# Performance work log

Hardware: AMD Instinct MI355X
Metric: run time of the kernel (lower is better)

The kernel has to match this reference:

```python
import jax, jax.numpy as jnp
import numpy as np

NUM_BITS = 10
D_MODEL = 256
D_INNER = 512                      # expand=2 * hidden
D_STATE = 64
N_HEADS = 8                        # D_INNER // head_dim(64)
HEAD_DIM = 64
CONV_DIM = D_INNER + 2 * D_STATE   # 640
D_PROJ = D_INNER + CONV_DIM + N_HEADS  # 1160
KERNEL = 4
EPS = 1e-5
N_TOKENS = 16384


def _hilbert_code(coords):
    # coords: (N,3) int32 in [0, 2**NUM_BITS); Skilling's AxesToTranspose + bit interleave
    n = 3
    x = [coords[:, i] for i in range(n)]
    M = 1 << (NUM_BITS - 1)
    Q = M
    while Q > 1:
        P = Q - 1
        for i in range(n):
            cond = (x[i] & Q) > 0
            t = (x[0] ^ x[i]) & P
            x0_new = jnp.where(cond, x[0] ^ P, x[0] ^ t)
            xi_new = jnp.where(cond, x[i], x[i] ^ t)
            x[0] = x0_new
            if i > 0:
                x[i] = xi_new
        Q >>= 1
    for i in range(1, n):
        x[i] = x[i] ^ x[i - 1]
    t = jnp.zeros_like(x[0])
    Q = M
    while Q > 1:
        t = jnp.where((x[n - 1] & Q) > 0, t ^ (Q - 1), t)
        Q >>= 1
    x = [xi ^ t for xi in x]
    code = jnp.zeros_like(x[0])
    for b in range(NUM_BITS - 1, -1, -1):
        for i in range(n):
            code = (code << 1) | ((x[i] >> b) & 1)
    return code


def _serialized_orders(query_pos):
    # quantize to a 2**NUM_BITS grid, Hilbert-encode, sort ('hilbert' and 'hilbert-trans' = x/y swapped)
    pmin = query_pos.min(0)
    pmax = query_pos.max(0)
    g = ((query_pos - pmin) / (pmax - pmin + 1e-6) * (2 ** NUM_BITS - 1))
    g = jnp.clip(g, 0, 2 ** NUM_BITS - 1).astype(jnp.int32)
    orders, inverses = [], []
    for perm in ((0, 1, 2), (1, 0, 2)):
        code = _hilbert_code(g[:, jnp.array(perm)])
        o = jnp.argsort(code)
        orders.append(o)
        inverses.append(jnp.argsort(o))
    return orders, inverses


def _ln(x, w, b):
    m = x.mean(-1, keepdims=True)
    xc = x - m
    return xc * jax.lax.rsqrt(jnp.mean(xc * xc, -1, keepdims=True) + EPS) * w + b


def _mamba2(x, p):
    # x: (B, L, D_MODEL)
    B, L, _ = x.shape
    zxbcdt = x @ p['in_proj']                           # (B,L,1160)
    gate = zxbcdt[..., :D_INNER]
    xBC = zxbcdt[..., D_INNER:D_INNER + CONV_DIM]
    dt = zxbcdt[..., D_INNER + CONV_DIM:]               # (B,L,H)
    # causal depthwise conv over time
    xc = jnp.moveaxis(xBC, -1, 1)                       # (B,C,L)
    xc = jax.lax.conv_general_dilated(
        xc, p['conv_w'][:, None, :], window_strides=(1,),
        padding=[(KERNEL - 1, 0)], dimension_numbers=('NCH', 'OIH', 'NCH'),
        feature_group_count=CONV_DIM)
    xc = xc + p['conv_b'][None, :, None]
    xBC = jax.nn.silu(jnp.moveaxis(xc, 1, -1))          # (B,L,C)
    xs = xBC[..., :D_INNER].reshape(B, L, N_HEADS, HEAD_DIM)
    Bm = xBC[..., D_INNER:D_INNER + D_STATE]            # (B,L,S), n_groups=1 broadcast over heads
    Cm = xBC[..., D_INNER + D_STATE:]                   # (B,L,S)
    dt = jax.nn.softplus(dt + p['dt_bias'])             # (B,L,H)
    A = -jnp.exp(p['A_log'])                            # (H,)
    dA = jnp.exp(dt * A)                                # (B,L,H)

    def step(h, inp):
        dA_t, dt_t, x_t, B_t, C_t = inp                 # (B,H),(B,H),(B,H,P),(B,S),(B,S)
        h = h * dA_t[..., None, None] + (dt_t[..., None] * x_t)[..., None] * B_t[:, None, None, :]
        y = jnp.einsum('bhps,bs->bhp', h, C_t)
        return h, y

    tm = lambda a: jnp.moveaxis(a, 1, 0)
    h0 = jnp.zeros((B, N_HEADS, HEAD_DIM, D_STATE), x.dtype)
    _, ys = jax.lax.scan(step, h0, (tm(dA), tm(dt), tm(xs), tm(Bm), tm(Cm)))
    y = jnp.moveaxis(ys, 0, 1) + p['D'][None, None, :, None] * xs   # (B,L,H,P) + D skip
    y = y.reshape(B, L, D_INNER)
    # gated RMSNorm (MambaRMSNormGated)
    y = y * jax.nn.silu(gate)
    y = y * jax.lax.rsqrt(jnp.mean(y * y, -1, keepdims=True) + EPS) * p['norm_w']
    return y @ p['out_proj']                            # (B,L,D_MODEL)


def _forward(query, query_pos, pre_w, pre_b, fin_w, fin_b, layer_params):
    orders, invs = _serialized_orders(query_pos)
    q = query
    for p in layer_params:
        shortcut = q
        qn = _ln(q, pre_w, pre_b)
        stacked = jnp.stack([qn[orders[0]], qn[orders[1]]])   # (2, N, d) multi-path serialization
        y = _mamba2(stacked, p)
        q = shortcut + (y[0][invs[0]] + y[1][invs[1]]) * 0.5  # scatter back + average paths
        q = _ln(q, fin_w, fin_b)
    return q


def setup_inputs() -> dict:
    key = jax.random.key(0)
    ks = jax.random.split(key, 24)
    inp = {
        'query': jax.random.normal(ks[0], (N_TOKENS, D_MODEL), jnp.float32),
        'query_pos': jax.random.uniform(ks[1], (N_TOKENS, 3), jnp.float32),
        'pre_w': jnp.ones((D_MODEL,), jnp.float32),
        'pre_b': jnp.zeros((D_MODEL,), jnp.float32),
        'fin_w': jnp.ones((D_MODEL,), jnp.float32),
        'fin_b': jnp.zeros((D_MODEL,), jnp.float32),
    }
    for i in range(2):
        k = jax.random.split(ks[2 + i], 6)
        inp[f'in_proj{i}'] = jax.random.normal(k[0], (D_MODEL, D_PROJ), jnp.float32) * 0.02
        inp[f'conv_w{i}'] = jax.random.normal(k[1], (CONV_DIM, KERNEL), jnp.float32) * 0.2
        inp[f'conv_b{i}'] = jnp.zeros((CONV_DIM,), jnp.float32)
        inp[f'dt_bias{i}'] = jax.random.uniform(k[2], (N_HEADS,), jnp.float32, -4.0, -1.0)
        inp[f'A_log{i}'] = jnp.log(jnp.arange(1, N_HEADS + 1, dtype=jnp.float32))
        inp[f'D{i}'] = jnp.ones((N_HEADS,), jnp.float32)
        inp[f'norm_w{i}'] = jnp.ones((D_INNER,), jnp.float32)
        inp[f'out_proj{i}'] = jax.random.normal(k[3], (D_INNER, D_MODEL), jnp.float32) * 0.02
    return inp


def reference(query, query_pos, pre_w, pre_b, fin_w, fin_b,
              in_proj0, conv_w0, conv_b0, dt_bias0, A_log0, D0, norm_w0, out_proj0,
              in_proj1, conv_w1, conv_b1, dt_bias1, A_log1, D1, norm_w1, out_proj1):
    layer_params = [
        dict(in_proj=in_proj0, conv_w=conv_w0, conv_b=conv_b0, dt_bias=dt_bias0,
             A_log=A_log0, D=D0, norm_w=norm_w0, out_proj=out_proj0),
        dict(in_proj=in_proj1, conv_w=conv_w1, conv_b=conv_b1, dt_bias=dt_bias1,
             A_log=A_log1, D=D1, norm_w=norm_w1, out_proj=out_proj1),
    ]
    return _forward(query, query_pos, pre_w, pre_b, fin_w, fin_b, layer_params)
```

## Files before the change

### kernel.cpp

```cpp
#include <hip/hip_runtime.h>
#include <stdint.h>

#define L_TOK 16384
#define DM 256
#define DI 512
#define DS 64
#define NH 8
#define HD 64
#define CD 640
#define DP 1160
#define CHUNK 64
#define NC 256
#define EPSF 1e-5f

typedef __attribute__((ext_vector_type(8))) short short8;
typedef __attribute__((ext_vector_type(4))) float f32x4;

#define GLL16(gp, lp) __builtin_amdgcn_global_load_lds((const __attribute__((address_space(1))) void*)(gp), (__attribute__((address_space(3))) void*)(lp), 16, 0, 0)

__device__ __forceinline__ float warp_sum(float v) {
  v += __shfl_xor(v, 1, 64);
  v += __shfl_xor(v, 2, 64);
  v += __shfl_xor(v, 4, 64);
  v += __shfl_xor(v, 8, 64);
  v += __shfl_xor(v, 16, 64);
  v += __shfl_xor(v, 32, 64);
  return v;
}

__device__ __forceinline__ float fexp(float x) { return __expf(x); }
__device__ __forceinline__ float fsilu(float x) { return x * __builtin_amdgcn_rcpf(1.0f + __expf(-x)); }
__device__ __forceinline__ float siluf(float x) { return x / (1.0f + expf(-x)); }

__device__ __forceinline__ unsigned short f2bf(float f) {
  unsigned int u = __float_as_uint(f);
  unsigned int r = (u + 0x7FFFu + ((u >> 16) & 1u)) >> 16;
  return (unsigned short)r;
}
__device__ __forceinline__ float bf2f(unsigned short u) {
  return __uint_as_float(((unsigned int)u) << 16);
}


__global__ __launch_bounds__(256) void minmax_part(const float* __restrict__ pos, float* __restrict__ part) {
  __shared__ float sm[6][4];
  int tid = threadIdx.x;
  int t = blockIdx.x*256 + tid;
  float a = pos[t*3+0], b = pos[t*3+1], c = pos[t*3+2];
  float mn0=a, mn1=b, mn2=c, mx0=a, mx1=b, mx2=c;
  #pragma unroll
  for (int d = 1; d < 64; d <<= 1) {
    mn0=fminf(mn0,__shfl_xor(mn0,d,64));
    mn1=fminf(mn1,__shfl_xor(mn1,d,64));
    mn2=fminf(mn2,__shfl_xor(mn2,d,64));
    mx0=fmaxf(mx0,__shfl_xor(mx0,d,64));
    mx1=fmaxf(mx1,__shfl_xor(mx1,d,64));
    mx2=fmaxf(mx2,__shfl_xor(mx2,d,64));
  }
  if ((tid & 63) == 0) {
    int w = tid >> 6;
    sm[0][w]=mn0; sm[1][w]=mn1; sm[2][w]=mn2;
    sm[3][w]=mx0; sm[4][w]=mx1; sm[5][w]=mx2;
  }
  __syncthreads();
  if (tid < 6) {
    float r = sm[tid][0];
    if (tid < 3) { r=fminf(r,sm[tid][1]); r=fminf(r,sm[tid][2]); r=fminf(r,sm[tid][3]); }
    else         { r=fmaxf(r,sm[tid][1]); r=fmaxf(r,sm[tid][2]); r=fmaxf(r,sm[tid][3]); }
    part[blockIdx.x*6 + tid] = r;
  }
}

__global__ __launch_bounds__(64) void minmax_final(const float* __restrict__ part, float* __restrict__ pmm) {
  int tid = threadIdx.x;
  const float* p = part + tid*6;
  float mn0=p[0], mn1=p[1], mn2=p[2], mx0=p[3], mx1=p[4], mx2=p[5];
  #pragma unroll
  for (int d = 1; d < 64; d <<= 1) {
    mn0=fminf(mn0,__shfl_xor(mn0,d,64));
    mn1=fminf(mn1,__shfl_xor(mn1,d,64));
    mn2=fminf(mn2,__shfl_xor(mn2,d,64));
    mx0=fmaxf(mx0,__shfl_xor(mx0,d,64));
    mx1=fmaxf(mx1,__shfl_xor(mx1,d,64));
    mx2=fmaxf(mx2,__shfl_xor(mx2,d,64));
  }
  if (tid == 0) {
    pmm[0]=mn0; pmm[1]=mn1; pmm[2]=mn2;
    pmm[3]=mx0; pmm[4]=mx1; pmm[5]=mx2;
  }
}

__device__ unsigned int hilbert3(unsigned int a, unsigned int b, unsigned int c) {
  unsigned int x0 = a, x1 = b, x2 = c;
  for (unsigned int Q = 512u; Q > 1u; Q >>= 1) {
    unsigned int P = Q - 1u;
    { if (x0 & Q) x0 ^= P; }
    {
      unsigned int t = (x0 ^ x1) & P;
      if (x1 & Q) { x0 ^= P; }
      else { x0 ^= t; x1 ^= t; }
    }
    {
      unsigned int t = (x0 ^ x2) & P;
      if (x2 & Q) { x0 ^= P; }
      else { x0 ^= t; x2 ^= t; }
    }
  }
  x1 ^= x0; x2 ^= x1;
  unsigned int tt = 0;
  for (unsigned int Q = 512u; Q > 1u; Q >>= 1)
    if (x2 & Q) tt ^= (Q - 1u);
  x0 ^= tt; x1 ^= tt; x2 ^= tt;
  unsigned int code = 0;
  #pragma unroll
  for (int bb = 9; bb >= 0; --bb) {
    code = (code << 1) | ((x0 >> bb) & 1u);
    code = (code << 1) | ((x1 >> bb) & 1u);
    code = (code << 1) | ((x2 >> bb) & 1u);
  }
  return code;
}

__global__ __launch_bounds__(256) void hilbert_kernel(const float* __restrict__ pos, const float* __restrict__ pmm,
                                                      unsigned long long* __restrict__ keys) {
  int t = blockIdx.x*256 + threadIdx.x;
  if (t >= L_TOK) return;
  unsigned int g[3];
  #pragma unroll
  for (int d = 0; d < 3; ++d) {
    float v = (pos[t*3+d] - pmm[d]) / (pmm[3+d] - pmm[d] + 1e-6f) * 1023.0f;
    v = fminf(fmaxf(v, 0.0f), 1023.0f);
    g[d] = (unsigned int)(int)v;
  }
  unsigned int ca = hilbert3(g[0], g[1], g[2]);
  unsigned int cb = hilbert3(g[1], g[0], g[2]);
  keys[t]         = ((unsigned long long)ca << 14) | (unsigned long long)t;
  keys[L_TOK + t] = ((unsigned long long)cb << 14) | (unsigned long long)t;
}

__global__ __launch_bounds__(256) void rank_partial(const unsigned long long* __restrict__ keys,
                                                    unsigned int* __restrict__ partial) {
  __shared__ unsigned long long tile[512];
  int arr = blockIdx.y, ks = blockIdx.z;
  const unsigned long long* k = keys + (size_t)arr * L_TOK;
  int qbase = blockIdx.x*1024 + threadIdx.x;
  unsigned long long q[4];
  #pragma unroll
  for (int i = 0; i < 4; ++i) q[i] = k[qbase + 256*i];
  const unsigned long long* src = k + ks*512;
  #pragma unroll
  for (int t = 0; t < 2; ++t) tile[threadIdx.x + 256*t] = src[threadIdx.x + 256*t];
  __syncthreads();
  unsigned int r[4] = {};
  const ulonglong2* t2 = (const ulonglong2*)tile;
  #pragma unroll 4
  for (int j = 0; j < 256; ++j) {
    ulonglong2 v = t2[j];
    #pragma unroll
    for (int i = 0; i < 4; ++i) {
      r[i] += (v.x < q[i]) ? 1u : 0u;
      r[i] += (v.y < q[i]) ? 1u : 0u;
    }
  }
  #pragma unroll
  for (int i = 0; i < 4; ++i)
    partial[(size_t)(ks*2 + arr)*L_TOK + qbase + 256*i] = r[i];
}

__global__ __launch_bounds__(256) void rank_scatter(const unsigned long long* __restrict__ keys,
                                                    const unsigned int* __restrict__ partial,
                                                    unsigned int* __restrict__ ord,
                                                    unsigned int* __restrict__ inv) {
  int i = blockIdx.x*256 + threadIdx.x;
  int arr = i >> 14;
  int qi = i & (L_TOK - 1);
  unsigned int r = 0;
  #pragma unroll
  for (int ks = 0; ks < 32; ++ks) r += partial[(size_t)(ks*2 + arr)*L_TOK + qi];
  unsigned int tok = (unsigned int)(keys[i] & 0x3FFFu);
  ord[(size_t)arr*L_TOK + r] = tok;
  inv[(size_t)arr*L_TOK + tok] = r;
}


__global__ __launch_bounds__(256) void ln_kernel(const float* __restrict__ in, float* __restrict__ out,
                                                 unsigned short* __restrict__ outbf,
                                                 const float* __restrict__ w, const float* __restrict__ b) {
  int row = blockIdx.x*4 + (threadIdx.x >> 6);
  int lane = threadIdx.x & 63;
  const float4 v = *(const float4*)(in + (size_t)row*DM + lane*4);
  float s = v.x + v.y + v.z + v.w;
  float mean = warp_sum(s) * (1.0f/DM);
  float4 xc = make_float4(v.x-mean, v.y-mean, v.z-mean, v.w-mean);
  float ss = xc.x*xc.x + xc.y*xc.y + xc.z*xc.z + xc.w*xc.w;
  ss = warp_sum(ss) * (1.0f/DM);
  float inv = rsqrtf(ss + EPSF);
  const float4 w4 = *(const float4*)(w + lane*4);
  const float4 b4 = *(const float4*)(b + lane*4);
  float4 o;
  o.x = xc.x*inv*w4.x + b4.x;
  o.y = xc.y*inv*w4.y + b4.y;
  o.z = xc.z*inv*w4.z + b4.z;
  o.w = xc.w*inv*w4.w + b4.w;
  *(float4*)(out + (size_t)row*DM + lane*4) = o;
  if (outbf) {
    ushort4 ob = make_ushort4(f2bf(o.x), f2bf(o.y), f2bf(o.z), f2bf(o.w));
    *(ushort4*)(outbf + (size_t)row*DM + lane*4) = ob;
  }
}

__global__ __launch_bounds__(256) void lnfuse_kernel(float* __restrict__ io,
                                                     float* __restrict__ qn, unsigned short* __restrict__ qnbf,
                                                     const float* __restrict__ fw, const float* __restrict__ fb,
                                                     const float* __restrict__ pw, const float* __restrict__ pb) {
  int row = blockIdx.x*4 + (threadIdx.x >> 6);
  int lane = threadIdx.x & 63;
  const float4 v = *(const float4*)(io + (size_t)row*DM + lane*4);
  float s = v.x + v.y + v.z + v.w;
  float mean = warp_sum(s) * (1.0f/DM);
  float4 xc = make_float4(v.x-mean, v.y-mean, v.z-mean, v.w-mean);
  float ss = xc.x*xc.x + xc.y*xc.y + xc.z*xc.z + xc.w*xc.w;
  ss = warp_sum(ss) * (1.0f/DM);
  float inv = rsqrtf(ss + EPSF);
  const float4 w4 = *(const float4*)(fw + lane*4);
  const float4 b4 = *(const float4*)(fb + lane*4);
  float4 o;
  o.x = xc.x*inv*w4.x + b4.x;
  o.y = xc.y*inv*w4.y + b4.y;
  o.z = xc.z*inv*w4.z + b4.z;
  o.w = xc.w*inv*w4.w + b4.w;
  *(float4*)(io + (size_t)row*DM + lane*4) = o;
  if (qn) {
    float s2 = o.x + o.y + o.z + o.w;
    float mean2 = warp_sum(s2) * (1.0f/DM);
    float4 x2 = make_float4(o.x-mean2, o.y-mean2, o.z-mean2, o.w-mean2);
    float ss2 = x2.x*x2.x + x2.y*x2.y + x2.z*x2.z + x2.w*x2.w;
    ss2 = warp_sum(ss2) * (1.0f/DM);
    float inv2 = rsqrtf(ss2 + EPSF);
    const float4 pw4 = *(const float4*)(pw + lane*4);
    const float4 pb4 = *(const float4*)(pb + lane*4);
    float4 qv;
    qv.x = x2.x*inv2*pw4.x + pb4.x;
    qv.y = x2.y*inv2*pw4.y + pb4.y;
    qv.z = x2.z*inv2*pw4.z + pb4.z;
    qv.w = x2.w*inv2*pw4.w + pb4.w;
    *(float4*)(qn + (size_t)row*DM + lane*4) = qv;
    ushort4 qb = make_ushort4(f2bf(qv.x), f2bf(qv.y), f2bf(qv.z), f2bf(qv.w));
    *(ushort4*)(qnbf + (size_t)row*DM + lane*4) = qb;
  }
}


__global__ __launch_bounds__(256) void tcvt_both(const float* __restrict__ Wi, const float* __restrict__ Wo,
                                                 const float* __restrict__ nw,
                                                 unsigned short* __restrict__ WtA, unsigned short* __restrict__ WtO) {
  int idx = blockIdx.x*256 + threadIdx.x;
  if (idx < 1152*DM) {
    int n = idx >> 8, k = idx & 255;
    WtA[idx] = f2bf(Wi[(size_t)k*DP + n]);
  } else {
    int j = idx - 1152*DM;
    int n = j >> 9, k = j & 511;
    WtO[j] = f2bf(Wo[(size_t)k*DM + n] * nw[k]);
  }
}


__global__ __launch_bounds__(256) void gemm_in2(const unsigned short* __restrict__ Abf,
                                                const unsigned short* __restrict__ Wt,
                                                const unsigned int* __restrict__ ord,
                                                unsigned short* __restrict__ gate_nat,
                                                unsigned short* __restrict__ bcraw,
                                                unsigned short* __restrict__ xTg) {
  __shared__ unsigned short Alds[128*64];
  __shared__ unsigned short Blds[128*64];
  int tid = threadIdx.x, lane = tid & 63, w = tid >> 6;
  int bid = blockIdx.x;
  bool natp = bid < 640;
  int rb, cb, dir = 0, wcol0;
  if (natp) {
    int xcd = bid & 7, g = bid >> 3;
    rb = (xcd*16 + g/5)*128;
    cb = (g % 5)*128;
    wcol0 = cb;
  } else {
    int id = bid - 640;
    dir = id >> 9;
    int b = id & 511;
    int xcd = b & 7, g = b >> 3;
    rb = (xcd*16 + g/4)*128;
    cb = (g % 4)*128;
    wcol0 = DI + cb;
  }
  int wm = (w & 1)*64, wn = (w >> 1)*64;
  const unsigned int* ordp = ord + (size_t)dir*L_TOK;
  const unsigned short* pA[4]; const unsigned short* pB[4];
  unsigned short* dA[4]; unsigned short* dB[4];
  #pragma unroll
  for (int s = 0; s < 4; ++s) {
    int inst = w*4 + s;
    int r = inst*8 + (lane >> 3);
    int cA = (lane & 7) ^ (r & 7);
    int arow = natp ? (rb + r) : (int)ordp[rb + r];
    pA[s] = Abf + (size_t)arow*DM + cA*8;
    pB[s] = Wt + (size_t)(wcol0 + r)*DM + cA*8;
    dA[s] = &Alds[inst*512];
    dB[s] = &Blds[inst*512];
  }
  f32x4 zero = {0.f, 0.f, 0.f, 0.f};
  f32x4 acc[4][4];
  #pragma unroll
  for (int i = 0; i < 4; ++i)
    #pragma unroll
    for (int j = 0; j < 4; ++j) acc[i][j] = zero;
  int t = lane & 15, q = lane >> 4;
  for (int k0 = 0; k0 < DM; k0 += 64) {
    #pragma unroll
    for (int s = 0; s < 4; ++s) GLL16(pA[s] + k0, dA[s]);
    #pragma unroll
    for (int s = 0; s < 4; ++s) GLL16(pB[s] + k0, dB[s]);
    __syncthreads();
    #pragma unroll
    for (int ks = 0; ks < 2; ++ks) {
      short8 af[4], bfr[4];
      int cc = ks*4 + q;
      #pragma unroll
      for (int i = 0; i < 4; ++i) {
        int rr = wm + 16*i + t;
        af[i] = *(const short8*)&Alds[rr*64 + ((cc ^ (rr & 7))*8)];
      }
      #pragma unroll
      for (int j = 0; j < 4; ++j) {
        int rr = wn + 16*j + t;
        bfr[j] = *(const short8*)&Blds[rr*64 + ((cc ^ (rr & 7))*8)];
      }
      #pragma unroll
      for (int i = 0; i < 4; ++i)
        #pragma unroll
        for (int j = 0; j < 4; ++j)
          acc[i][j] = __builtin_amdgcn_mfma_f32_16x16x32_bf16(af[i], bfr[j], acc[i][j], 0, 0, 0);
    }
    __syncthreads();
  }
  if (natp) {
    unsigned short* dst; int ld;
    if (cb < DI) { dst = gate_nat + cb; ld = DI; }
    else         { dst = bcraw + (cb - DI); ld = 128; }
    #pragma unroll
    for (int i = 0; i < 4; ++i) {
      int rowb = rb + wm + 16*i + q*4;
      #pragma unroll
      for (int j = 0; j < 4; ++j) {
        int col = wn + 16*j + t;
        #pragma unroll
        for (int r = 0; r < 4; ++r)
          dst[(size_t)(rowb + r)*ld + col] = f2bf(acc[i][j][r]);
      }
    }
  } else {
    #pragma unroll
    for (int i = 0; i < 4; ++i) {
      int rowb = rb + wm + 16*i + q*4;
      #pragma unroll
      for (int j = 0; j < 4; ++j) {
        int col = wn + 16*j + t;
        ushort4 o = make_ushort4(f2bf(acc[i][j][0]), f2bf(acc[i][j][1]),
                                 f2bf(acc[i][j][2]), f2bf(acc[i][j][3]));
        *(ushort4*)(xTg + (size_t)(cb + col)*(2*L_TOK) + (size_t)dir*L_TOK + rowb) = o;
      }
    }
  }
}


__global__ __launch_bounds__(256) void gemm_out_gather(const unsigned short* __restrict__ ybuf,
                                                       const unsigned short* __restrict__ Wt,
                                                       const unsigned int* __restrict__ inv,
                                                       const float* __restrict__ rms_acc,
                                                       const float* __restrict__ shortcut,
                                                       float* __restrict__ out) {
  __shared__ unsigned short Alds[2*64*64];
  __shared__ unsigned short Blds[128*64];
  int tid = threadIdx.x, lane = tid & 63, w = tid >> 6;
  int bid = blockIdx.x;
  int xcd = bid & 7, g = bid >> 3;
  int rb = (xcd*32 + (g >> 1))*64;
  int cb = (g & 1)*128;
  int wm = (w & 1)*32, wn = (w >> 1)*64;
  const unsigned short* pA0[2]; const unsigned short* pA1[2];
  unsigned short* dA0[2]; unsigned short* dA1[2];
  const unsigned short* pB[4]; unsigned short* dB[4];
  #pragma unroll
  for (int s = 0; s < 2; ++s) {
    int inst = w*2 + s;
    int r = inst*8 + (lane >> 3);
    int cA = (lane & 7) ^ (r & 7);
    int tok = rb + r;
    pA0[s] = ybuf + (size_t)inv[tok]*DI + cA*8;
    pA1[s] = ybuf + (size_t)L_TOK*DI + (size_t)inv[L_TOK + tok]*DI + cA*8;
    dA0[s] = &Alds[inst*512];
    dA1[s] = &Alds[4096 + inst*512];
  }
  #pragma unroll
  for (int s = 0; s < 4; ++s) {
    int inst = w*4 + s;
    int r = inst*8 + (lane >> 3);
    int cA = (lane & 7) ^ (r & 7);
    pB[s] = Wt + (size_t)(cb + r)*DI + cA*8;
    dB[s] = &Blds[inst*512];
  }
  f32x4 zero = {0.f, 0.f, 0.f, 0.f};
  f32x4 acc0[2][4], acc1[2][4];
  #pragma unroll
  for (int i = 0; i < 2; ++i)
    #pragma unroll
    for (int j = 0; j < 4; ++j) { acc0[i][j] = zero; acc1[i][j] = zero; }
  int t = lane & 15, q = lane >> 4;
  for (int k0 = 0; k0 < DI; k0 += 64) {
    #pragma unroll
    for (int s = 0; s < 2; ++s) { GLL16(pA0[s] + k0, dA0[s]); GLL16(pA1[s] + k0, dA1[s]); }
    #pragma unroll
    for (int s = 0; s < 4; ++s) GLL16(pB[s] + k0, dB[s]);
    __syncthreads();
    #pragma unroll
    for (int ks = 0; ks < 2; ++ks) {
      short8 af0[2], af1[2], bfr[4];
      int cc = ks*4 + q;
      #pragma unroll
      for (int i = 0; i < 2; ++i) {
        int rr = wm + 16*i + t;
        int off = rr*64 + ((cc ^ (rr & 7))*8);
        af0[i] = *(const short8*)&Alds[off];
        af1[i] = *(const short8*)&Alds[4096 + off];
      }
      #pragma unroll
      for (int j = 0; j < 4; ++j) {
        int rr = wn + 16*j + t;
        bfr[j] = *(const short8*)&Blds[rr*64 + ((cc ^ (rr & 7))*8)];
      }
      #pragma unroll
      for (int i = 0; i < 2; ++i)
        #pragma unroll
        for (int j = 0; j < 4; ++j) {
          acc0[i][j] = __builtin_amdgcn_mfma_f32_16x16x32_bf16(af0[i], bfr[j], acc0[i][j], 0, 0, 0);
          acc1[i][j] = __builtin_amdgcn_mfma_f32_16x16x32_bf16(af1[i], bfr[j], acc1[i][j], 0, 0, 0);
        }
    }
    __syncthreads();
  }
  #pragma unroll
  for (int i = 0; i < 2; ++i) {
    #pragma unroll
    for (int r = 0; r < 4; ++r) {
      int row = rb + wm + 16*i + q*4 + r;
      float ir0 = rsqrtf(rms_acc[row]*(1.0f/DI) + EPSF);
      float ir1 = rsqrtf(rms_acc[L_TOK + row]*(1.0f/DI) + EPSF);
      const float* sp = shortcut + (size_t)row*DM + cb;
      float* op = out + (size_t)row*DM + cb;
      #pragma unroll
      for (int j = 0; j < 4; ++j) {
        int col = wn + 16*j + t;
        op[col] = sp[col] + 0.5f*(ir0*acc0[i][j][r] + ir1*acc1[i][j][r]);
      }
    }
  }
}


__global__ __launch_bounds__(256) void dtconv(const float* __restrict__ qn, const float* __restrict__ W,
                                              const float* __restrict__ dt_bias, float* __restrict__ dtb,
                                              float* __restrict__ rms_acc,
                                              const unsigned short* __restrict__ bcraw,
                                              const float* __restrict__ cw, const float* __restrict__ cbias,
                                              const unsigned int* __restrict__ ord,
                                              unsigned short* __restrict__ bcswz,
                                              unsigned short* __restrict__ bcswzA) {
  __shared__ unsigned short smem[131*64];
  int tid = threadIdx.x;
  int bx = blockIdx.x;
  if (bx < 512) {
    int gid = bx*256 + tid;
    if (gid < 2*L_TOK) rms_acc[gid] = 0.f;
    float* Wl = (float*)smem;
    {
      const float* wp = W + (size_t)tid*DP + (DI + CD);
      float4 wa = *(const float4*)wp;
      float4 wb = *(const float4*)(wp + 4);
      int off = tid*8 + (tid >> 5)*4;
      *(float4*)&Wl[off]     = wa;
      *(float4*)&Wl[off + 4] = wb;
    }
    __syncthreads();
    int lane = tid & 63, w = tid >> 6;
    int r = bx*32 + w*8 + (lane >> 3);
    int kg = lane & 7;
    const float* qp = qn + (size_t)r*DM + kg*32;
    float acc[8] = {};
    #pragma unroll
    for (int i = 0; i < 8; ++i) {
      float4 q4 = *(const float4*)(qp + i*4);
      float qv[4] = {q4.x, q4.y, q4.z, q4.w};
      #pragma unroll
      for (int e = 0; e < 4; ++e) {
        int k = kg*32 + i*4 + e;
        int off = k*8 + kg*4;
        float4 wa = *(const float4*)&Wl[off];
        float4 wb = *(const float4*)&Wl[off + 4];
        acc[0] = fmaf(qv[e], wa.x, acc[0]);
        acc[1] = fmaf(qv[e], wa.y, acc[1]);
        acc[2] = fmaf(qv[e], wa.z, acc[2]);
        acc[3] = fmaf(qv[e], wa.w, acc[3]);
        acc[4] = fmaf(qv[e], wb.x, acc[4]);
        acc[5] = fmaf(qv[e], wb.y, acc[5]);
        acc[6] = fmaf(qv[e], wb.z, acc[6]);
        acc[7] = fmaf(qv[e], wb.w, acc[7]);
      }
    }
    #pragma unroll
    for (int h = 0; h < 8; ++h) {
      acc[h] += __shfl_xor(acc[h], 8, 64);
      acc[h] += __shfl_xor(acc[h], 16, 64);
      acc[h] += __shfl_xor(acc[h], 32, 64);
    }
    float v = 0.f;
    #pragma unroll
    for (int h = 0; h < 8; ++h) if (kg == h) v = acc[h];
    v += dt_bias[kg];
    float sp = (v > 0.0f) ? (v + log1pf(__expf(-v))) : log1pf(__expf(v));
    dtb[(size_t)r*NH + kg] = sp;
  } else {
    int cid = bx - 512;
    int half = cid & 1, ty = (cid >> 1) & 127, dir = cid >> 8;
    unsigned short* tile = smem;
    const unsigned int* ordp = ord + (size_t)dir*L_TOK;
    int ch0 = DI + half*64;
    int co0 = half*64;
    int t0 = ty*128;
    for (int cc = tid; cc < 131*8; cc += 256) {
      int r = cc >> 3, cgc = cc & 7;
      int t = t0 - 3 + r;
      short8 v = {0,0,0,0,0,0,0,0};
      if (t >= 0) v = *(const short8*)(bcraw + (size_t)ordp[t]*128 + co0 + cgc*8);
      *(short8*)&tile[r*64 + ((cgc ^ (r & 7))*8)] = v;
    }
    int cg = tid & 7, tp = tid >> 3;
    int ch = ch0 + cg*8;
    float wv[8][4];
    float bias[8];
    #pragma unroll
    for (int e = 0; e < 8; ++e) {
      float4 c4 = *(const float4*)(cw + (ch + e)*4);
      wv[e][0] = c4.x; wv[e][1] = c4.y; wv[e][2] = c4.z; wv[e][3] = c4.w;
    }
    {
      float4 b0 = *(const float4*)(cbias + ch);
      float4 b1 = *(const float4*)(cbias + ch + 4);
      bias[0]=b0.x; bias[1]=b0.y; bias[2]=b0.z; bias[3]=b0.w;
      bias[4]=b1.x; bias[5]=b1.y; bias[6]=b1.z; bias[7]=b1.w;
    }
    __syncthreads();
    #pragma unroll
    for (int tk = 0; tk < 4; ++tk) {
      int rel = tp + 32*tk;
      float acc[8];
      #pragma unroll
      for (int e = 0; e < 8; ++e) acc[e] = bias[e];
      #pragma unroll
      for (int k = 0; k < 4; ++k) {
        int r = rel + k;
        short8 v = *(const short8*)&tile[r*64 + ((cg ^ (r & 7))*8)];
        #pragma unroll
        for (int e = 0; e < 8; ++e)
          acc[e] = fmaf(wv[e][k], bf2f((unsigned short)v[e]), acc[e]);
      }
      short8 o;
      #pragma unroll
      for (int e = 0; e < 8; ++e) o[e] = (short)f2bf(fsilu(acc[e]));
      int T = t0 + rel;
      int chn = T >> 6, tl = T & 63;
      unsigned short* tb = bcswz + ((size_t)((dir*NC + chn)*2 + half))*4096;
      *(short8*)(tb + tl*64 + ((cg ^ (tl & 7))*8)) = o;
      if (half == 0) {
        unsigned short* ta = bcswzA + ((size_t)(dir*NC + chn))*4096;
        #pragma unroll
        for (int e = 0; e < 8; ++e) {
          int s5 = cg*8 + e;
          ta[s5*64 + (((tl >> 3) ^ (s5 & 7))*8) + (tl & 7)] = (unsigned short)o[e];
        }
      }
    }
  }
}


__global__ __launch_bounds__(256) void phaseA_mfma(const unsigned short* __restrict__ xTg,
                                                   const unsigned short* __restrict__ bcswzA,
                                                   const float* __restrict__ cw, const float* __restrict__ cbias,
                                                   const float* __restrict__ dtb, const float* __restrict__ A_log,
                                                   const unsigned int* __restrict__ ord,
                                                   unsigned short* __restrict__ S, float* __restrict__ P,
                                                   unsigned short* __restrict__ xsT) {
  int c = blockIdx.x, h = blockIdx.y, dir = blockIdx.z, tid = threadIdx.x;
  int lane = tid & 63, w = tid >> 6;
  int hh = dir*NH + h;
  __shared__ unsigned short xT[64*64];
  __shared__ unsigned short Bt[64*64];
  __shared__ float wgt[64];
  int c0 = c*CHUNK;
  float Ah = -expf(A_log[h]);
  const unsigned short* bA = bcswzA + ((size_t)(dir*NC + c))*4096;
  #pragma unroll
  for (int s = 0; s < 2; ++s) {
    int inst = w*2 + s;
    GLL16(bA + (size_t)inst*512 + lane*8, &Bt[inst*512]);
  }
  if (tid < 64) {
    unsigned int tok = ord[(size_t)dir*L_TOK + c0 + tid];
    float dtv = dtb[(size_t)tok*NH + h];
    float v = dtv*Ah;
    float s = v;
    #pragma unroll
    for (int d = 1; d < 64; d <<= 1) {
      float u = __shfl_down(s, d, 64);
      s += (tid + d < 64) ? u : 0.f;
    }
    wgt[tid] = dtv*fexp(s - v);
    if (tid == 0) P[hh*NC + c] = fexp(s);
  }
  __syncthreads();
  unsigned short* xpg = xsT + ((size_t)(hh*NC + c))*4096;
  #pragma unroll
  for (int i = 0; i < 2; ++i) {
    int q = tid + 256*i;
    int p = q >> 3, tg = q & 7;
    int sw8 = (tg ^ (p & 7))*8;
    const unsigned short* xrow = xTg + (size_t)(h*HD + p)*(2*L_TOK) + (size_t)dir*L_TOK;
    int tb = c0 + tg*8;
    short8 cur = *(const short8*)(xrow + tb);
    short8 prv = {0,0,0,0,0,0,0,0};
    if (tb >= 8) prv = *(const short8*)(xrow + tb - 8);
    float4 w4 = *(const float4*)(cw + (size_t)(h*HD + p)*4);
    float bb = cbias[h*HD + p];
    float xv[11];
    xv[0] = bf2f((unsigned short)prv[5]);
    xv[1] = bf2f((unsigned short)prv[6]);
    xv[2] = bf2f((unsigned short)prv[7]);
    #pragma unroll
    for (int k = 0; k < 8; ++k) xv[3+k] = bf2f((unsigned short)cur[k]);
    short8 raw, wtd;
    #pragma unroll
    for (int k = 0; k < 8; ++k) {
      float a = bb + w4.x*xv[k] + w4.y*xv[k+1] + w4.z*xv[k+2] + w4.w*xv[k+3];
      unsigned short rbf = f2bf(fsilu(a));
      raw[k] = (short)rbf;
      wtd[k] = (short)f2bf(bf2f(rbf)*wgt[tg*8 + k]);
    }
    *(short8*)(xpg + p*64 + sw8) = raw;
    *(short8*)&xT[p*64 + sw8] = wtd;
  }
  __syncthreads();
  int t16 = lane & 15, q4 = lane >> 4;
  f32x4 zero = {0.f,0.f,0.f,0.f};
  f32x4 acc[4];
  #pragma unroll
  for (int j = 0; j < 4; ++j) acc[j] = zero;
  #pragma unroll
  for (int ks = 0; ks < 2; ++ks) {
    int rowA = 16*w + t16;
    short8 a = *(const short8*)&xT[rowA*64 + (((ks*4 + q4) ^ (rowA & 7))*8)];
    #pragma unroll
    for (int j = 0; j < 4; ++j) {
      int rowB = 16*j + t16;
      short8 b = *(const short8*)&Bt[rowB*64 + (((ks*4 + q4) ^ (rowB & 7))*8)];
      acc[j] = __builtin_amdgcn_mfma_f32_16x16x32_bf16(a, b, acc[j], 0, 0, 0);
    }
  }
  unsigned short* Sp = S + ((size_t)(hh*NC + c))*4096;
  #pragma unroll
  for (int j = 0; j < 4; ++j)
    #pragma unroll
    for (int r = 0; r < 4; ++r) {
      int row = 16*w + q4*4 + r;
      int cg2 = 2*j + (t16 >> 3);
      Sp[(size_t)row*64 + (((cg2 ^ (row & 7)) << 3) | (t16 & 7))] = f2bf(acc[j][r]);
    }
}


__global__ __launch_bounds__(128) void phaseB_scan(unsigned short* __restrict__ S, const float* __restrict__ P) {
  __shared__ float Pl[NC];
  int b = blockIdx.x;
  int hh = b >> 4;
  int e2 = (b & 15)*128 + threadIdx.x;
  for (int i = threadIdx.x; i < NC; i += 128) Pl[i] = P[hh*NC + i];
  __syncthreads();
  unsigned int* base = (unsigned int*)(S + ((size_t)hh*NC)*4096) + e2;
  float hx = 0.f, hy = 0.f;
  #pragma unroll 1
  for (int k0 = 0; k0 < NC; k0 += 16) {
    unsigned int v[16];
    #pragma unroll
    for (int u = 0; u < 16; ++u) v[u] = base[(size_t)(k0+u)*2048];
    #pragma unroll
    for (int u = 0; u < 16; ++u) {
      float p = Pl[k0+u];
      unsigned int old = v[u];
      base[(size_t)(k0+u)*2048] = (unsigned int)f2bf(hx) | ((unsigned int)f2bf(hy) << 16);
      hx = p*hx + bf2f((unsigned short)(old & 0xffffu));
      hy = p*hy + bf2f((unsigned short)(old >> 16));
    }
  }
}

__global__ __launch_bounds__(256) void phaseC_mfma(const unsigned short* __restrict__ bcswz,
                                                   const unsigned short* __restrict__ xsT,
                                                   const unsigned short* __restrict__ gate_nat,
                                                   const float* __restrict__ dtb, const float* __restrict__ A_log,
                                                   const float* __restrict__ Dp,
                                                   const unsigned int* __restrict__ ord,
                                                   const unsigned short* __restrict__ S,
                                                   unsigned short* __restrict__ ybuf,
                                                   float* __restrict__ rms_acc) {
  int c = blockIdx.x, h = blockIdx.y, dir = blockIdx.z, tid = threadIdx.x;
  int lane = tid & 63, w = tid >> 6;
  int hh = dir*NH + h;
  unsigned short* y = ybuf + (size_t)dir*L_TOK*DI;
  __shared__ __align__(16) unsigned short smemT[4*4096];
  __shared__ float dts[64], pl[64], pe[64];
  unsigned short* Cl  = smemT;
  unsigned short* Bl  = smemT + 4096;
  unsigned short* h0l = smemT + 8192;
  unsigned short* xT  = smemT + 12288;
  float* fT = (float*)(smemT + 8192);
  int c0 = c*CHUNK;
  float Ah = -expf(A_log[h]);
  float Dh = Dp[h];
  const unsigned short* Sp = S + ((size_t)(hh*NC + c))*4096;
  const unsigned short* xp = xsT + ((size_t)(hh*NC + c))*4096;
  const unsigned short* Bg = bcswz + ((size_t)((dir*NC + c)*2 + 0))*4096;
  const unsigned short* Cg = bcswz + ((size_t)((dir*NC + c)*2 + 1))*4096;
  #pragma unroll
  for (int s = 0; s < 2; ++s) {
    int inst = w*2 + s;
    GLL16(Sp + (size_t)inst*512 + lane*8, &h0l[inst*512]);
    GLL16(xp + (size_t)inst*512 + lane*8, &xT[inst*512]);
    GLL16(Bg + (size_t)inst*512 + lane*8, &Bl[inst*512]);
    GLL16(Cg + (size_t)inst*512 + lane*8, &Cl[inst*512]);
  }
  int erow = tid >> 2;
  int ech0 = (tid & 3) * 16;
  unsigned int etok = ord[(size_t)dir*L_TOK + c0 + erow];
  const unsigned short* gp = gate_nat + (size_t)etok*DI + h*HD + ech0;
  short8 g0 = *(const short8*)gp;
  short8 g1 = *(const short8*)(gp + 8);
  if (tid < 64) {
    unsigned int tok = ord[(size_t)dir*L_TOK + c0 + tid];
    float dtv = dtb[(size_t)tok*NH + h];
    dts[tid] = dtv;
    float v = dtv*Ah;
    float s = v;
    #pragma unroll
    for (int d = 1; d < 64; d <<= 1) {
      float u = __shfl_up(s, d, 64);
      s += (tid >= d) ? u : 0.f;
    }
    pl[tid] = s;
    pe[tid] = fexp(s);
  }
  __syncthreads();
  int t16 = lane & 15, q4 = lane >> 4;
  int t0 = 16*w;
  f32x4 zero = {0.f,0.f,0.f,0.f};
  f32x4 accG[4], accY[4];
  #pragma unroll
  for (int j = 0; j < 4; ++j) { accG[j] = zero; accY[j] = zero; }
  #pragma unroll
  for (int ks = 0; ks < 2; ++ks) {
    int rowA = t0 + t16;
    short8 a = *(const short8*)&Cl[rowA*64 + (((ks*4 + q4) ^ (rowA & 7))*8)];
    #pragma unroll
    for (int j = 0; j < 4; ++j) {
      int rowB = 16*j + t16;
      int off = rowB*64 + (((ks*4 + q4) ^ (rowB & 7))*8);
      accG[j] = __builtin_amdgcn_mfma_f32_16x16x32_bf16(a, *(const short8*)&Bl[off], accG[j], 0, 0, 0);
      accY[j] = __builtin_amdgcn_mfma_f32_16x16x32_bf16(a, *(const short8*)&h0l[off], accY[j], 0, 0, 0);
    }
  }
  #pragma unroll
  for (int j = 0; j < 4; ++j) {
    #pragma unroll
    for (int r = 0; r < 4; ++r) {
      int t = t0 + q4*4 + r;
      int s = 16*j + t16;
      float v = 0.f;
      if (s <= t) {
        v = accG[j][r] * dts[s] * fexp(pl[t] - pl[s]);
        if (s == t) v += Dh;
      }
      Cl[t*64 + (((s >> 3) ^ (t & 7))*8 + (s & 7))] = f2bf(v);
    }
  }
  #pragma unroll
  for (int j = 0; j < 4; ++j)
    #pragma unroll
    for (int r = 0; r < 4; ++r)
      accY[j][r] *= pe[t0 + q4*4 + r];
  #pragma unroll
  for (int ks = 0; ks < 2; ++ks) {
    int rowA = t0 + t16;
    short8 a = *(const short8*)&Cl[rowA*64 + (((ks*4 + q4) ^ (rowA & 7))*8)];
    #pragma unroll
    for (int j = 0; j < 4; ++j) {
      int rowB = 16*j + t16;
      short8 b = *(const short8*)&xT[rowB*64 + (((ks*4 + q4) ^ (rowB & 7))*8)];
      accY[j] = __builtin_amdgcn_mfma_f32_16x16x32_bf16(a, b, accY[j], 0, 0, 0);
    }
  }
  __syncthreads();
  #pragma unroll
  for (int j = 0; j < 4; ++j)
    #pragma unroll
    for (int r = 0; r < 4; ++r) {
      int t = t0 + q4*4 + r;
      int p = 16*j + t16;
      fT[t*64 + (p ^ (q4 << 4))] = accY[j][r];
    }
  __syncthreads();
  {
    int swz = ((erow >> 2) & 3) << 4;
    const float* fr = &fT[erow*64 + (ech0 ^ swz)];
    float4 a0 = *(const float4*)(fr);
    float4 a1 = *(const float4*)(fr + 4);
    float4 a2 = *(const float4*)(fr + 8);
    float4 a3 = *(const float4*)(fr + 12);
    float fv[16] = {a0.x,a0.y,a0.z,a0.w, a1.x,a1.y,a1.z,a1.w,
                    a2.x,a2.y,a2.z,a2.w, a3.x,a3.y,a3.z,a3.w};
    float sq = 0.f;
    short8 o0, o1;
    #pragma unroll
    for (int e = 0; e < 8; ++e) {
      float v0 = fv[e]   * fsilu(bf2f((unsigned short)g0[e]));
      float v1 = fv[8+e] * fsilu(bf2f((unsigned short)g1[e]));
      o0[e] = (short)f2bf(v0);
      o1[e] = (short)f2bf(v1);
      sq += v0*v0 + v1*v1;
    }
    unsigned short* yp = y + (size_t)(c0 + erow)*DI + h*HD + ech0;
    *(short8*)yp = o0;
    *(short8*)(yp + 8) = o1;
    sq += __shfl_xor(sq, 1, 64);
    sq += __shfl_xor(sq, 2, 64);
    if ((tid & 3) == 0) atomicAdd(&rms_acc[(size_t)dir*L_TOK + etok], sq);
  }
}

__global__ void fill_debug(float* out, float v) {
  int i = blockIdx.x*256 + threadIdx.x;
  if (i < L_TOK*DM) out[i] = v;
}


extern "C" void kernel_launch(void* const* d_in, const int* in_sizes, int n_in,
                              void* d_out, int out_size, void* d_ws, size_t ws_size,
                              hipStream_t stream) {
  const float* query = (const float*)d_in[0];
  const float* qpos  = (const float*)d_in[1];
  const float* pre_w = (const float*)d_in[2];
  const float* pre_b = (const float*)d_in[3];
  const float* fin_w = (const float*)d_in[4];
  const float* fin_b = (const float*)d_in[5];
  float* out = (float*)d_out;

  char* ws = (char*)d_ws;
  size_t off = 0;
  auto alloc = [&](size_t bytes) -> void* {
    void* p = ws + off;
    off += (bytes + 255) & ~(size_t)255;
    return p;
  };
  unsigned long long* keys = (unsigned long long*)alloc((size_t)2*L_TOK*8);
  unsigned int* ord = (unsigned int*)alloc((size_t)2*L_TOK*4);
  unsigned int* inv = (unsigned int*)alloc((size_t)2*L_TOK*4);
  unsigned int* rpart = (unsigned int*)alloc((size_t)32*2*L_TOK*4);
  float* pmm  = (float*)alloc(256);
  float* mmpart = (float*)alloc((size_t)64*6*4);
  float* qn   = (float*)alloc((size_t)L_TOK*DM*4);
  unsigned short* qnbf = (unsigned short*)alloc((size_t)L_TOK*DM*2);
  unsigned short* gate_nat = (unsigned short*)alloc((size_t)L_TOK*DI*2);
  unsigned short* xTg    = (unsigned short*)alloc((size_t)512*2*L_TOK*2);
  unsigned short* bcraw  = (unsigned short*)alloc((size_t)L_TOK*128*2);
  unsigned short* bcswz  = (unsigned short*)alloc((size_t)2*NC*2*4096*2);
  unsigned short* bcswzA = (unsigned short*)alloc((size_t)2*NC*4096*2);
  unsigned short* ybuf   = (unsigned short*)alloc((size_t)2*L_TOK*DI*2);
  float* dtb  = (float*)alloc((size_t)L_TOK*NH*4);
  float* rms_acc = (float*)alloc((size_t)2*L_TOK*4);
  unsigned short* Sbuf = (unsigned short*)alloc((size_t)2*NH*NC*4096*2);
  unsigned short* xsT  = (unsigned short*)alloc((size_t)2*NH*NC*4096*2);
  float* Pbuf = (float*)alloc((size_t)2*NH*NC*4);
  unsigned short* WtA = (unsigned short*)alloc((size_t)1152*DM*2);
  unsigned short* WtO = (unsigned short*)alloc((size_t)DM*DI*2);
  if (off > ws_size) {
    fill_debug<<<(L_TOK*DM + 255)/256, 256, 0, stream>>>(out, (float)(ws_size >> 20));
    return;
  }

  minmax_part<<<64, 256, 0, stream>>>(qpos, mmpart);
  minmax_final<<<1, 64, 0, stream>>>(mmpart, pmm);
  hilbert_kernel<<<L_TOK/256, 256, 0, stream>>>(qpos, pmm, keys);
  rank_partial<<<dim3(16, 2, 32), 256, 0, stream>>>(keys, rpart);
  rank_scatter<<<(2*L_TOK)/256, 256, 0, stream>>>(keys, rpart, ord, inv);

  for (int l = 0; l < 2; ++l) {
    int base = 6 + 8*l;
    const float* in_proj  = (const float*)d_in[base+0];
    const float* conv_w   = (const float*)d_in[base+1];
    const float* conv_b   = (const float*)d_in[base+2];
    const float* dt_bias  = (const float*)d_in[base+3];
    const float* A_log    = (const float*)d_in[base+4];
    const float* Dp       = (const float*)d_in[base+5];
    const float* norm_w   = (const float*)d_in[base+6];
    const float* out_proj = (const float*)d_in[base+7];

    if (l == 0)
      ln_kernel<<<L_TOK/4, 256, 0, stream>>>(query, qn, qnbf, pre_w, pre_b);
    tcvt_both<<<(1152*DM + DM*DI)/256, 256, 0, stream>>>(in_proj, out_proj, norm_w, WtA, WtO);
    gemm_in2<<<1664, 256, 0, stream>>>(qnbf, WtA, ord, gate_nat, bcraw, xTg);
    dtconv<<<1024, 256, 0, stream>>>(qn, in_proj, dt_bias, dtb, rms_acc,
                                     bcraw, conv_w, conv_b, ord, bcswz, bcswzA);
    phaseA_mfma<<<dim3(NC, NH, 2), 256, 0, stream>>>(xTg, bcswzA, conv_w, conv_b, dtb, A_log, ord, Sbuf, Pbuf, xsT);
    phaseB_scan<<<256, 128, 0, stream>>>(Sbuf, Pbuf);
    phaseC_mfma<<<dim3(NC, NH, 2), 256, 0, stream>>>(bcswz, xsT, gate_nat, dtb, A_log, Dp, ord, Sbuf, ybuf, rms_acc);
    gemm_out_gather<<<512, 256, 0, stream>>>(ybuf, WtO, inv, rms_acc,
                                             l ? (const float*)out : query, out);
    if (l == 0)
      lnfuse_kernel<<<L_TOK/4, 256, 0, stream>>>(out, qn, qnbf, fin_w, fin_b, pre_w, pre_b);
    else
      lnfuse_kernel<<<L_TOK/4, 256, 0, stream>>>(out, nullptr, nullptr, fin_w, fin_b, pre_w, pre_b);
  }
}
```

Baseline: 470.8 us.

## Sort key tiles for binary-search ranking, fuse minmax, tile weight transpose

Adds a bitonic sort of each 512-key tile so rank_partial can binary-search instead of comparing every query against all 512 keys, cutting the ranking work from linear to logarithmic per tile. The final min/max reduction is folded into hilbert_kernel, which removes one launch. The weight transpose/convert kernel now goes through an LDS tile with vectorized loads and stores instead of strided scalar reads. The conv halo in phaseA is built from cross-lane shuffles rather than a second global load. The changes add an extra sort kernel and buffer, and put redundant reduction work in every hilbert block.

```diff
diff --git a/kernel.cpp b/kernel.cpp
--- a/kernel.cpp
+++ b/kernel.cpp
@@ -30,7 +30,6 @@
 
 __device__ __forceinline__ float fexp(float x) { return __expf(x); }
 __device__ __forceinline__ float fsilu(float x) { return x * __builtin_amdgcn_rcpf(1.0f + __expf(-x)); }
-__device__ __forceinline__ float siluf(float x) { return x / (1.0f + expf(-x)); }
 
 __device__ __forceinline__ unsigned short f2bf(float f) {
   unsigned int u = __float_as_uint(f);
@@ -68,25 +67,6 @@
     if (tid < 3) { r=fminf(r,sm[tid][1]); r=fminf(r,sm[tid][2]); r=fminf(r,sm[tid][3]); }
     else         { r=fmaxf(r,sm[tid][1]); r=fmaxf(r,sm[tid][2]); r=fmaxf(r,sm[tid][3]); }
     part[blockIdx.x*6 + tid] = r;
-  }
-}
-
-__global__ __launch_bounds__(64) void minmax_final(const float* __restrict__ part, float* __restrict__ pmm) {
-  int tid = threadIdx.x;
-  const float* p = part + tid*6;
-  float mn0=p[0], mn1=p[1], mn2=p[2], mx0=p[3], mx1=p[4], mx2=p[5];
-  #pragma unroll
-  for (int d = 1; d < 64; d <<= 1) {
-    mn0=fminf(mn0,__shfl_xor(mn0,d,64));
-    mn1=fminf(mn1,__shfl_xor(mn1,d,64));
-    mn2=fminf(mn2,__shfl_xor(mn2,d,64));
-    mx0=fmaxf(mx0,__shfl_xor(mx0,d,64));
-    mx1=fmaxf(mx1,__shfl_xor(mx1,d,64));
-    mx2=fmaxf(mx2,__shfl_xor(mx2,d,64));
-  }
-  if (tid == 0) {
-    pmm[0]=mn0; pmm[1]=mn1; pmm[2]=mn2;
-    pmm[3]=mx0; pmm[4]=mx1; pmm[5]=mx2;
   }
 }
 
@@ -121,14 +101,33 @@
   return code;
 }
 
-__global__ __launch_bounds__(256) void hilbert_kernel(const float* __restrict__ pos, const float* __restrict__ pmm,
+__global__ __launch_bounds__(256) void hilbert_kernel(const float* __restrict__ pos, const float* __restrict__ part,
                                                       unsigned long long* __restrict__ keys) {
-  int t = blockIdx.x*256 + threadIdx.x;
-  if (t >= L_TOK) return;
+  __shared__ float spmm[6];
+  int tid = threadIdx.x;
+  if (tid < 64) {
+    const float* p = part + tid*6;
+    float mn0=p[0], mn1=p[1], mn2=p[2], mx0=p[3], mx1=p[4], mx2=p[5];
+    #pragma unroll
+    for (int d = 1; d < 64; d <<= 1) {
+      mn0=fminf(mn0,__shfl_xor(mn0,d,64));
+      mn1=fminf(mn1,__shfl_xor(mn1,d,64));
+      mn2=fminf(mn2,__shfl_xor(mn2,d,64));
+      mx0=fmaxf(mx0,__shfl_xor(mx0,d,64));
+      mx1=fmaxf(mx1,__shfl_xor(mx1,d,64));
+      mx2=fmaxf(mx2,__shfl_xor(mx2,d,64));
+    }
+    if (tid == 0) {
+      spmm[0]=mn0; spmm[1]=mn1; spmm[2]=mn2;
+      spmm[3]=mx0; spmm[4]=mx1; spmm[5]=mx2;
+    }
+  }
+  __syncthreads();
+  int t = blockIdx.x*256 + tid;
   unsigned int g[3];
   #pragma unroll
   for (int d = 0; d < 3; ++d) {
-    float v = (pos[t*3+d] - pmm[d]) / (pmm[3+d] - pmm[d] + 1e-6f) * 1023.0f;
+    float v = (pos[t*3+d] - spmm[d]) / (spmm[3+d] - spmm[d] + 1e-6f) * 1023.0f;
     v = fminf(fmaxf(v, 0.0f), 1023.0f);
     g[d] = (unsigned int)(int)v;
   }
@@ -138,7 +137,35 @@
   keys[L_TOK + t] = ((unsigned long long)cb << 14) | (unsigned long long)t;
 }
 
+__global__ __launch_bounds__(256) void sort_tiles(const unsigned long long* __restrict__ keys,
+                                                  unsigned long long* __restrict__ skeys) {
+  __shared__ unsigned long long s[512];
+  int b = blockIdx.x, tid = threadIdx.x;
+  size_t base = (size_t)(b >> 5)*L_TOK + (size_t)(b & 31)*512;
+  s[tid]       = keys[base + tid];
+  s[tid + 256] = keys[base + tid + 256];
+  for (unsigned int k = 2; k <= 512; k <<= 1) {
+    for (unsigned int j = k >> 1; j > 0; j >>= 1) {
+      __syncthreads();
+      #pragma unroll
+      for (int h = 0; h < 2; ++h) {
+        int i = tid + 256*h;
+        int ixj = i ^ (int)j;
+        if (ixj > i) {
+          unsigned long long a = s[i], c = s[ixj];
+          bool up = ((i & (int)k) == 0);
+          if (up ? (a > c) : (a < c)) { s[i] = c; s[ixj] = a; }
+        }
+      }
+    }
+  }
+  __syncthreads();
+  skeys[base + tid]       = s[tid];
+  skeys[base + tid + 256] = s[tid + 256];
+}
+
 __global__ __launch_bounds__(256) void rank_partial(const unsigned long long* __restrict__ keys,
+                                                    const unsigned long long* __restrict__ skeys,
                                                     unsigned int* __restrict__ partial) {
   __shared__ unsigned long long tile[512];
   int arr = blockIdx.y, ks = blockIdx.z;
@@ -147,24 +174,19 @@
   unsigned long long q[4];
   #pragma unroll
   for (int i = 0; i < 4; ++i) q[i] = k[qbase + 256*i];
-  const unsigned long long* src = k + ks*512;
-  #pragma unroll
-  for (int t = 0; t < 2; ++t) tile[threadIdx.x + 256*t] = src[threadIdx.x + 256*t];
+  const unsigned long long* src = skeys + (size_t)arr*L_TOK + ks*512;
+  tile[threadIdx.x]       = src[threadIdx.x];
+  tile[threadIdx.x + 256] = src[threadIdx.x + 256];
   __syncthreads();
-  unsigned int r[4] = {};
-  const ulonglong2* t2 = (const ulonglong2*)tile;
-  #pragma unroll 4
-  for (int j = 0; j < 256; ++j) {
-    ulonglong2 v = t2[j];
-    #pragma unroll
-    for (int i = 0; i < 4; ++i) {
-      r[i] += (v.x < q[i]) ? 1u : 0u;
-      r[i] += (v.y < q[i]) ? 1u : 0u;
-    }
-  }
-  #pragma unroll
-  for (int i = 0; i < 4; ++i)
-    partial[(size_t)(ks*2 + arr)*L_TOK + qbase + 256*i] = r[i];
+  #pragma unroll
+  for (int i = 0; i < 4; ++i) {
+    unsigned int lo = 0;
+    #pragma unroll
+    for (unsigned int st = 256; st > 0; st >>= 1)
+      if (tile[lo + st - 1] < q[i]) lo += st;
+    lo += (tile[lo] < q[i]) ? 1u : 0u;
+    partial[(size_t)(ks*2 + arr)*L_TOK + qbase + 256*i] = lo;
+  }
 }
 
 __global__ __launch_bounds__(256) void rank_scatter(const unsigned long long* __restrict__ keys,
@@ -254,15 +276,51 @@
 __global__ __launch_bounds__(256) void tcvt_both(const float* __restrict__ Wi, const float* __restrict__ Wo,
                                                  const float* __restrict__ nw,
                                                  unsigned short* __restrict__ WtA, unsigned short* __restrict__ WtO) {
-  int idx = blockIdx.x*256 + threadIdx.x;
-  if (idx < 1152*DM) {
-    int n = idx >> 8, k = idx & 255;
-    WtA[idx] = f2bf(Wi[(size_t)k*DP + n]);
+  __shared__ float lds[64*65];
+  int b = blockIdx.x, tid = threadIdx.x;
+  const float* src; int srcld, n0, k0t, dstld; unsigned short* dst; bool useNw;
+  if (b < 72) {
+    int nt = b >> 2, kt = b & 3;
+    n0 = nt*64; k0t = kt*64;
+    src = Wi; srcld = DP; dst = WtA; dstld = 256; useNw = false;
   } else {
-    int j = idx - 1152*DM;
-    int n = j >> 9, k = j & 511;
-    WtO[j] = f2bf(Wo[(size_t)k*DM + n] * nw[k]);
-  }
+    int j = b - 72;
+    int nt = j >> 3, kt = j & 7;
+    n0 = nt*64; k0t = kt*64;
+    src = Wo; srcld = DM; dst = WtO; dstld = 512; useNw = true;
+  }
+  int nn = (tid & 15)*4, kk = tid >> 4;
+  #pragma unroll
+  for (int p = 0; p < 4; ++p) {
+    int k = kk + p*16;
+    float4 v = *(const float4*)(src + (size_t)(k0t + k)*srcld + n0 + nn);
+    lds[k*65 + nn]   = v.x;
+    lds[k*65 + nn+1] = v.y;
+    lds[k*65 + nn+2] = v.z;
+    lds[k*65 + nn+3] = v.w;
+  }
+  __syncthreads();
+  int n = tid >> 2, kq = (tid & 3)*16;
+  float nwv[16];
+  if (useNw) {
+    #pragma unroll
+    for (int e = 0; e < 16; e += 4) {
+      float4 t4 = *(const float4*)(nw + k0t + kq + e);
+      nwv[e]=t4.x; nwv[e+1]=t4.y; nwv[e+2]=t4.z; nwv[e+3]=t4.w;
+    }
+  } else {
+    #pragma unroll
+    for (int e = 0; e < 16; ++e) nwv[e] = 1.0f;
+  }
+  short8 o0, o1;
+  #pragma unroll
+  for (int e = 0; e < 8; ++e) {
+    o0[e] = (short)f2bf(lds[(kq+e)*65 + n] * nwv[e]);
+    o1[e] = (short)f2bf(lds[(kq+8+e)*65 + n] * nwv[8+e]);
+  }
+  unsigned short* dp = dst + (size_t)(n0 + n)*dstld + k0t + kq;
+  *(short8*)dp = o0;
+  *(short8*)(dp + 8) = o1;
 }
 
 
@@ -637,14 +695,24 @@
     const unsigned short* xrow = xTg + (size_t)(h*HD + p)*(2*L_TOK) + (size_t)dir*L_TOK;
     int tb = c0 + tg*8;
     short8 cur = *(const short8*)(xrow + tb);
-    short8 prv = {0,0,0,0,0,0,0,0};
-    if (tb >= 8) prv = *(const short8*)(xrow + tb - 8);
+    int sh5 = __shfl_up((int)(unsigned short)cur[5], 1, 64);
+    int sh6 = __shfl_up((int)(unsigned short)cur[6], 1, 64);
+    int sh7 = __shfl_up((int)(unsigned short)cur[7], 1, 64);
+    unsigned short b5 = 0, b6 = 0, b7 = 0;
+    if (tg == 0) {
+      if (tb >= 8) {
+        ushort4 pv = *(const ushort4*)(xrow + tb - 4);
+        b5 = pv.y; b6 = pv.z; b7 = pv.w;
+      }
+    } else {
+      b5 = (unsigned short)sh5; b6 = (unsigned short)sh6; b7 = (unsigned short)sh7;
+    }
     float4 w4 = *(const float4*)(cw + (size_t)(h*HD + p)*4);
     float bb = cbias[h*HD + p];
     float xv[11];
-    xv[0] = bf2f((unsigned short)prv[5]);
-    xv[1] = bf2f((unsigned short)prv[6]);
-    xv[2] = bf2f((unsigned short)prv[7]);
+    xv[0] = bf2f(b5);
+    xv[1] = bf2f(b6);
+    xv[2] = bf2f(b7);
     #pragma unroll
     for (int k = 0; k < 8; ++k) xv[3+k] = bf2f((unsigned short)cur[k]);
     short8 raw, wtd;
@@ -879,10 +947,10 @@
     return p;
   };
   unsigned long long* keys = (unsigned long long*)alloc((size_t)2*L_TOK*8);
+  unsigned long long* skeys = (unsigned long long*)alloc((size_t)2*L_TOK*8);
   unsigned int* ord = (unsigned int*)alloc((size_t)2*L_TOK*4);
   unsigned int* inv = (unsigned int*)alloc((size_t)2*L_TOK*4);
   unsigned int* rpart = (unsigned int*)alloc((size_t)32*2*L_TOK*4);
-  float* pmm  = (float*)alloc(256);
   float* mmpart = (float*)alloc((size_t)64*6*4);
   float* qn   = (float*)alloc((size_t)L_TOK*DM*4);
   unsigned short* qnbf = (unsigned short*)alloc((size_t)L_TOK*DM*2);
@@ -905,9 +973,9 @@
   }
 
   minmax_part<<<64, 256, 0, stream>>>(qpos, mmpart);
-  minmax_final<<<1, 64, 0, stream>>>(mmpart, pmm);
-  hilbert_kernel<<<L_TOK/256, 256, 0, stream>>>(qpos, pmm, keys);
-  rank_partial<<<dim3(16, 2, 32), 256, 0, stream>>>(keys, rpart);
+  hilbert_kernel<<<L_TOK/256, 256, 0, stream>>>(qpos, mmpart, keys);
+  sort_tiles<<<64, 256, 0, stream>>>(keys, skeys);
+  rank_partial<<<dim3(16, 2, 32), 256, 0, stream>>>(keys, skeys, rpart);
   rank_scatter<<<(2*L_TOK)/256, 256, 0, stream>>>(keys, rpart, ord, inv);
 
   for (int l = 0; l < 2; ++l) {
@@ -923,7 +991,7 @@
 
     if (l == 0)
       ln_kernel<<<L_TOK/4, 256, 0, stream>>>(query, qn, qnbf, pre_w, pre_b);
-    tcvt_both<<<(1152*DM + DM*DI)/256, 256, 0, stream>>>(in_proj, out_proj, norm_w, WtA, WtO);
+    tcvt_both<<<104, 256, 0, stream>>>(in_proj, out_proj, norm_w, WtA, WtO);
     gemm_in2<<<1664, 256, 0, stream>>>(qnbf, WtA, ord, gate_nat, bcraw, xTg);
     dtconv<<<1024, 256, 0, stream>>>(qn, in_proj, dt_bias, dtb, rms_acc,
                                      bcraw, conv_w, conv_b, ord, bcswz, bcswzA);
```

Result: faster. 444.4 us (-5.6%).
